# Kernel optimization log

Hardware: AMD Instinct MI355X
Metric: run time of the kernel (lower is better)

The kernel has to match this reference:

```python
import jax, jax.numpy as jnp
import numpy as np

HIDDEN = 128
HEADS = 8
HEAD_DIM = HIDDEN // HEADS


def setup_inputs() -> dict:
    key = jax.random.key(0)
    ks = jax.random.split(key, 10)
    B, V = 2, 768
    s = 1.0 / np.sqrt(HIDDEN)
    return {
        "x": jax.random.normal(ks[0], (B, V, HIDDEN), dtype=jnp.float32),
        "edge_gate": jax.random.uniform(ks[1], (B, V, V, HIDDEN), dtype=jnp.float32),
        "Wq": jax.random.normal(ks[2], (HIDDEN, HIDDEN), dtype=jnp.float32) * s,
        "bq": jnp.zeros((HIDDEN,), dtype=jnp.float32),
        "Wk": jax.random.normal(ks[3], (HIDDEN, HIDDEN), dtype=jnp.float32) * s,
        "bk": jnp.zeros((HIDDEN,), dtype=jnp.float32),
        "Wv": jax.random.normal(ks[4], (HIDDEN, HIDDEN), dtype=jnp.float32) * s,
        "bv": jnp.zeros((HIDDEN,), dtype=jnp.float32),
        "Wo": jax.random.normal(ks[5], (HIDDEN, HIDDEN), dtype=jnp.float32) * s,
        "bo": jnp.zeros((HIDDEN,), dtype=jnp.float32),
    }


def reference(x, edge_gate, Wq, bq, Wk, bk, Wv, bv, Wo, bo):
    B, V, H = x.shape
    nh, hd = HEADS, HEAD_DIM
    # torch Linear: y = x @ W.T + b
    q = (x @ Wq.T + bq).reshape(B, V, nh, hd).transpose(0, 2, 1, 3)  # (B,nh,V,hd)
    k = (x @ Wk.T + bk).reshape(B, V, nh, hd).transpose(0, 2, 1, 3)
    v = (x @ Wv.T + bv).reshape(B, V, nh, hd).transpose(0, 2, 1, 3)
    scores = jnp.einsum("bhqd,bhkd->bhqk", q, k) / jnp.sqrt(jnp.float32(hd))
    edge_mask = jnp.mean(edge_gate, axis=-1)[:, None]  # (B,1,V,V)
    weights = jax.nn.softmax(scores * edge_mask, axis=-1)
    attended = jnp.einsum("bhqk,bhkd->bhqd", weights, v)
    attended = attended.transpose(0, 2, 1, 3).reshape(B, V, H)
    return attended @ Wo.T + bo
```

## Files before the change

kernel.cpp:

```cpp
#include <hip/hip_runtime.h>
#include <math.h>

#define BB 2
#define VV 768
#define HID 128
#define NH 8
#define HD 16

#define QKV_BLOCKS 768
#define EDGE_BLOCKS 2048
#define EDGE_WAVES (EDGE_BLOCKS * 4)
#define NPAIR (BB * VV * VV / 2)
#define EDGE_ITERS (NPAIR / EDGE_WAVES)

__global__ __launch_bounds__(256) void fused_qkv_edgemean(
    const float* __restrict__ x, const float* __restrict__ eg,
    const float* __restrict__ Wq, const float* __restrict__ bq,
    const float* __restrict__ Wk, const float* __restrict__ bk,
    const float* __restrict__ Wv, const float* __restrict__ bv,
    float* __restrict__ qh, float* __restrict__ kh, float* __restrict__ vh,
    float* __restrict__ mask) {
    __shared__ float xs[2][HID];
    if (blockIdx.x < QKV_BLOCKS) {
        const int half = threadIdx.x >> 7;
        const int c    = threadIdx.x & 127;
        const int row  = blockIdx.x * 2 + half;
        xs[half][c] = x[row * HID + c];
        __syncthreads();
        const float4* xs4 = (const float4*)xs[half];
        const float4* wq4 = (const float4*)(Wq + c * HID);
        const float4* wk4 = (const float4*)(Wk + c * HID);
        const float4* wv4 = (const float4*)(Wv + c * HID);
        float aq = 0.f, ak = 0.f, av = 0.f;
#pragma unroll
        for (int k4 = 0; k4 < HID / 4; ++k4) {
            float4 xv = xs4[k4];
            float4 a = wq4[k4];
            aq += xv.x * a.x + xv.y * a.y + xv.z * a.z + xv.w * a.w;
            float4 bv2 = wk4[k4];
            ak += xv.x * bv2.x + xv.y * bv2.y + xv.z * bv2.z + xv.w * bv2.w;
            float4 cv = wv4[k4];
            av += xv.x * cv.x + xv.y * cv.y + xv.z * cv.z + xv.w * cv.w;
        }
        const int b = row / VV, vi = row - b * VV;
        const int idx = ((b * NH + (c >> 4)) * VV + vi) * HD + (c & 15);
        qh[idx] = aq + bq[c];
        kh[idx] = ak + bk[c];
        vh[idx] = av + bv[c];
    } else {
        const int lane = threadIdx.x & 63;
        const int w = (blockIdx.x - QKV_BLOCKS) * 4 + (threadIdx.x >> 6);
        const float4* eg4 = (const float4*)eg;
#pragma unroll 4
        for (int it = 0; it < EDGE_ITERS; ++it) {
            const int p = w + it * EDGE_WAVES;
            float4 v = eg4[(size_t)p * 64 + lane];
            float s = v.x + v.y + v.z + v.w;
            s += __shfl_xor(s, 1);
            s += __shfl_xor(s, 2);
            s += __shfl_xor(s, 4);
            s += __shfl_xor(s, 8);
            s += __shfl_xor(s, 16);
            if ((lane & 31) == 0)
                mask[p * 2 + (lane >> 5)] = s * (1.0f / 128.0f);
        }
    }
}

__global__ __launch_bounds__(256) void attn_kernel(
    const float* __restrict__ qh, const float* __restrict__ kh,
    const float* __restrict__ vh, const float* __restrict__ mask,
    float* __restrict__ att) {
    __shared__ float sc[4][VV];
    const int wid  = threadIdx.x >> 6;
    const int lane = threadIdx.x & 63;
    const int gw   = blockIdx.x * 4 + wid;
    const int qi   = gw % VV;
    const int bh   = gw / VV;
    const int b    = bh >> 3, h = bh & 7;

    const float4* qp = (const float4*)(qh + (size_t)(bh * VV + qi) * HD);
    const float4 q0 = qp[0], q1 = qp[1], q2 = qp[2], q3 = qp[3];

    const float* mrow  = mask + (size_t)(b * VV + qi) * VV;
    const float* kbase = kh + (size_t)bh * VV * HD;
    const float* vbase = vh + (size_t)bh * VV * HD;

    float m = -INFINITY;
#pragma unroll
    for (int t = 0; t < VV / 64; ++t) {
        const int j = lane + 64 * t;
        const float4* kp = (const float4*)(kbase + j * HD);
        float4 k0 = kp[0], k1 = kp[1], k2 = kp[2], k3 = kp[3];
        float dot = q0.x * k0.x + q0.y * k0.y + q0.z * k0.z + q0.w * k0.w
                  + q1.x * k1.x + q1.y * k1.y + q1.z * k1.z + q1.w * k1.w
                  + q2.x * k2.x + q2.y * k2.y + q2.z * k2.z + q2.w * k2.w
                  + q3.x * k3.x + q3.y * k3.y + q3.z * k3.z + q3.w * k3.w;
        float s = dot * 0.25f * mrow[j];
        sc[wid][j] = s;
        m = fmaxf(m, s);
    }
#pragma unroll
    for (int off = 1; off < 64; off <<= 1) m = fmaxf(m, __shfl_xor(m, off));

    float sum = 0.f;
    float acc[HD];
#pragma unroll
    for (int d = 0; d < HD; ++d) acc[d] = 0.f;
#pragma unroll
    for (int t = 0; t < VV / 64; ++t) {
        const int j = lane + 64 * t;
        float e = __expf(sc[wid][j] - m);
        sum += e;
        const float4* vp = (const float4*)(vbase + j * HD);
        float4 v0 = vp[0], v1 = vp[1], v2 = vp[2], v3 = vp[3];
        acc[0]  += e * v0.x; acc[1]  += e * v0.y; acc[2]  += e * v0.z; acc[3]  += e * v0.w;
        acc[4]  += e * v1.x; acc[5]  += e * v1.y; acc[6]  += e * v1.z; acc[7]  += e * v1.w;
        acc[8]  += e * v2.x; acc[9]  += e * v2.y; acc[10] += e * v2.z; acc[11] += e * v2.w;
        acc[12] += e * v3.x; acc[13] += e * v3.y; acc[14] += e * v3.z; acc[15] += e * v3.w;
    }
#pragma unroll
    for (int off = 1; off < 64; off <<= 1) sum += __shfl_xor(sum, off);

#pragma unroll
    for (int i = 0; i < 8; ++i) {
        float send = (lane & 1) ? acc[i] : acc[i + 8];
        float r = __shfl_xor(send, 1);
        acc[i] = ((lane & 1) ? acc[i + 8] : acc[i]) + r;
    }
#pragma unroll
    for (int i = 0; i < 4; ++i) {
        float send = (lane & 2) ? acc[i] : acc[i + 4];
        float r = __shfl_xor(send, 2);
        acc[i] = ((lane & 2) ? acc[i + 4] : acc[i]) + r;
    }
#pragma unroll
    for (int i = 0; i < 2; ++i) {
        float send = (lane & 4) ? acc[i] : acc[i + 2];
        float r = __shfl_xor(send, 4);
        acc[i] = ((lane & 4) ? acc[i + 2] : acc[i]) + r;
    }
    {
        float send = (lane & 8) ? acc[0] : acc[1];
        float r = __shfl_xor(send, 8);
        acc[0] = ((lane & 8) ? acc[1] : acc[0]) + r;
    }
    acc[0] += __shfl_xor(acc[0], 16);
    acc[0] += __shfl_xor(acc[0], 32);

    const float inv = 1.0f / sum;
    const int d = ((lane & 1) << 3) | ((lane & 2) << 1) | ((lane & 4) >> 1) | ((lane & 8) >> 3);
    if (lane < HD)
        att[(size_t)(b * VV + qi) * HID + h * HD + d] = acc[0] * inv;
}

__global__ __launch_bounds__(128) void outproj_kernel(
    const float* __restrict__ att, const float* __restrict__ Wo,
    const float* __restrict__ bo, float* __restrict__ out) {
    const int row = blockIdx.x;
    const int c   = threadIdx.x;
    __shared__ float xs[HID];
    xs[c] = att[row * HID + c];
    __syncthreads();
    const float4* xs4 = (const float4*)xs;
    const float4* wo4 = (const float4*)(Wo + c * HID);
    float a = 0.f;
#pragma unroll
    for (int k4 = 0; k4 < HID / 4; ++k4) {
        float4 xv = xs4[k4];
        float4 wv = wo4[k4];
        a += xv.x * wv.x + xv.y * wv.y + xv.z * wv.z + xv.w * wv.w;
    }
    out[row * HID + c] = a + bo[c];
}

extern "C" void kernel_launch(void* const* d_in, const int* in_sizes, int n_in,
                              void* d_out, int out_size, void* d_ws, size_t ws_size,
                              hipStream_t stream) {
    const float* x  = (const float*)d_in[0];
    const float* eg = (const float*)d_in[1];
    const float* Wq = (const float*)d_in[2];
    const float* bq = (const float*)d_in[3];
    const float* Wk = (const float*)d_in[4];
    const float* bk = (const float*)d_in[5];
    const float* Wv = (const float*)d_in[6];
    const float* bv = (const float*)d_in[7];
    const float* Wo = (const float*)d_in[8];
    const float* bo = (const float*)d_in[9];
    float* out = (float*)d_out;

    float* ws   = (float*)d_ws;
    float* mask = ws;
    float* qh   = mask + (size_t)BB * VV * VV;
    float* kh   = qh + (size_t)BB * VV * HID;
    float* vh   = kh + (size_t)BB * VV * HID;
    float* att  = vh + (size_t)BB * VV * HID;

    hipLaunchKernelGGL(fused_qkv_edgemean, dim3(QKV_BLOCKS + EDGE_BLOCKS), dim3(256), 0, stream,
                       x, eg, Wq, bq, Wk, bk, Wv, bv, qh, kh, vh, mask);
    hipLaunchKernelGGL(attn_kernel, dim3(BB * NH * VV / 4), dim3(256), 0, stream,
                       qh, kh, vh, mask, att);
    hipLaunchKernelGGL(outproj_kernel, dim3(BB * VV), dim3(128), 0, stream,
                       att, Wo, bo, out);
}
```

Measured before the change: 243.5 us.

## Process two queries per wave in attention and give each edge-mean wave a contiguous chunk

```diff
diff --git a/kernel.cpp b/kernel.cpp
--- a/kernel.cpp
+++ b/kernel.cpp
@@ -48,21 +48,23 @@
         kh[idx] = ak + bk[c];
         vh[idx] = av + bv[c];
     } else {
-        const int lane = threadIdx.x & 63;
+        const int l = threadIdx.x & 63;
         const int w = (blockIdx.x - QKV_BLOCKS) * 4 + (threadIdx.x >> 6);
         const float4* eg4 = (const float4*)eg;
+        const size_t wbase = (size_t)w * (EDGE_ITERS * 64);
 #pragma unroll 4
         for (int it = 0; it < EDGE_ITERS; ++it) {
-            const int p = w + it * EDGE_WAVES;
-            float4 v = eg4[(size_t)p * 64 + lane];
-            float s = v.x + v.y + v.z + v.w;
+            float4 v = eg4[wbase + it * 64 + l];
+            float s = (v.x + v.y) + (v.z + v.w);
             s += __shfl_xor(s, 1);
             s += __shfl_xor(s, 2);
             s += __shfl_xor(s, 4);
             s += __shfl_xor(s, 8);
             s += __shfl_xor(s, 16);
-            if ((lane & 31) == 0)
-                mask[p * 2 + (lane >> 5)] = s * (1.0f / 128.0f);
+            if ((l & 31) == 0) {
+                const int p = w * EDGE_ITERS + it;
+                mask[p * 2 + (l >> 5)] = s * (1.0f / 128.0f);
+            }
         }
     }
 }
@@ -71,87 +73,125 @@
     const float* __restrict__ qh, const float* __restrict__ kh,
     const float* __restrict__ vh, const float* __restrict__ mask,
     float* __restrict__ att) {
-    __shared__ float sc[4][VV];
+    __shared__ float sc[4][2][VV];
     const int wid  = threadIdx.x >> 6;
     const int lane = threadIdx.x & 63;
     const int gw   = blockIdx.x * 4 + wid;
-    const int qi   = gw % VV;
-    const int bh   = gw / VV;
+    const int pr   = gw % (VV / 2);
+    const int bh   = gw / (VV / 2);
     const int b    = bh >> 3, h = bh & 7;
-
-    const float4* qp = (const float4*)(qh + (size_t)(bh * VV + qi) * HD);
-    const float4 q0 = qp[0], q1 = qp[1], q2 = qp[2], q3 = qp[3];
-
-    const float* mrow  = mask + (size_t)(b * VV + qi) * VV;
+    const int q0i  = pr * 2, q1i = q0i + 1;
+
+    const float4* qp0 = (const float4*)(qh + ((size_t)bh * VV + q0i) * HD);
+    const float4 qa0 = qp0[0], qa1 = qp0[1], qa2 = qp0[2], qa3 = qp0[3];
+    const float4* qp1 = (const float4*)(qh + ((size_t)bh * VV + q1i) * HD);
+    const float4 qb0 = qp1[0], qb1 = qp1[1], qb2 = qp1[2], qb3 = qp1[3];
+
+    const float* mrow0 = mask + ((size_t)b * VV + q0i) * VV;
+    const float* mrow1 = mrow0 + VV;
     const float* kbase = kh + (size_t)bh * VV * HD;
     const float* vbase = vh + (size_t)bh * VV * HD;
 
-    float m = -INFINITY;
+    float m0 = -INFINITY, m1 = -INFINITY;
 #pragma unroll
     for (int t = 0; t < VV / 64; ++t) {
         const int j = lane + 64 * t;
         const float4* kp = (const float4*)(kbase + j * HD);
         float4 k0 = kp[0], k1 = kp[1], k2 = kp[2], k3 = kp[3];
-        float dot = q0.x * k0.x + q0.y * k0.y + q0.z * k0.z + q0.w * k0.w
-                  + q1.x * k1.x + q1.y * k1.y + q1.z * k1.z + q1.w * k1.w
-                  + q2.x * k2.x + q2.y * k2.y + q2.z * k2.z + q2.w * k2.w
-                  + q3.x * k3.x + q3.y * k3.y + q3.z * k3.z + q3.w * k3.w;
-        float s = dot * 0.25f * mrow[j];
-        sc[wid][j] = s;
-        m = fmaxf(m, s);
-    }
-#pragma unroll
-    for (int off = 1; off < 64; off <<= 1) m = fmaxf(m, __shfl_xor(m, off));
-
-    float sum = 0.f;
-    float acc[HD];
-#pragma unroll
-    for (int d = 0; d < HD; ++d) acc[d] = 0.f;
+        float d0 = qa0.x * k0.x + qa0.y * k0.y + qa0.z * k0.z + qa0.w * k0.w
+                 + qa1.x * k1.x + qa1.y * k1.y + qa1.z * k1.z + qa1.w * k1.w
+                 + qa2.x * k2.x + qa2.y * k2.y + qa2.z * k2.z + qa2.w * k2.w
+                 + qa3.x * k3.x + qa3.y * k3.y + qa3.z * k3.z + qa3.w * k3.w;
+        float d1 = qb0.x * k0.x + qb0.y * k0.y + qb0.z * k0.z + qb0.w * k0.w
+                 + qb1.x * k1.x + qb1.y * k1.y + qb1.z * k1.z + qb1.w * k1.w
+                 + qb2.x * k2.x + qb2.y * k2.y + qb2.z * k2.z + qb2.w * k2.w
+                 + qb3.x * k3.x + qb3.y * k3.y + qb3.z * k3.z + qb3.w * k3.w;
+        float s0 = d0 * 0.25f * mrow0[j];
+        float s1 = d1 * 0.25f * mrow1[j];
+        sc[wid][0][j] = s0;
+        sc[wid][1][j] = s1;
+        m0 = fmaxf(m0, s0);
+        m1 = fmaxf(m1, s1);
+    }
+#pragma unroll
+    for (int off = 1; off < 64; off <<= 1) {
+        m0 = fmaxf(m0, __shfl_xor(m0, off));
+        m1 = fmaxf(m1, __shfl_xor(m1, off));
+    }
+
+    float sum0 = 0.f, sum1 = 0.f;
+    float acc0[HD], acc1[HD];
+#pragma unroll
+    for (int d = 0; d < HD; ++d) { acc0[d] = 0.f; acc1[d] = 0.f; }
 #pragma unroll
     for (int t = 0; t < VV / 64; ++t) {
         const int j = lane + 64 * t;
-        float e = __expf(sc[wid][j] - m);
-        sum += e;
+        float e0 = __expf(sc[wid][0][j] - m0);
+        float e1 = __expf(sc[wid][1][j] - m1);
+        sum0 += e0;
+        sum1 += e1;
         const float4* vp = (const float4*)(vbase + j * HD);
         float4 v0 = vp[0], v1 = vp[1], v2 = vp[2], v3 = vp[3];
-        acc[0]  += e * v0.x; acc[1]  += e * v0.y; acc[2]  += e * v0.z; acc[3]  += e * v0.w;
-        acc[4]  += e * v1.x; acc[5]  += e * v1.y; acc[6]  += e * v1.z; acc[7]  += e * v1.w;
-        acc[8]  += e * v2.x; acc[9]  += e * v2.y; acc[10] += e * v2.z; acc[11] += e * v2.w;
-        acc[12] += e * v3.x; acc[13] += e * v3.y; acc[14] += e * v3.z; acc[15] += e * v3.w;
-    }
-#pragma unroll
-    for (int off = 1; off < 64; off <<= 1) sum += __shfl_xor(sum, off);
+        acc0[0]  += e0 * v0.x; acc0[1]  += e0 * v0.y; acc0[2]  += e0 * v0.z; acc0[3]  += e0 * v0.w;
+        acc0[4]  += e0 * v1.x; acc0[5]  += e0 * v1.y; acc0[6]  += e0 * v1.z; acc0[7]  += e0 * v1.w;
+        acc0[8]  += e0 * v2.x; acc0[9]  += e0 * v2.y; acc0[10] += e0 * v2.z; acc0[11] += e0 * v2.w;
+        acc0[12] += e0 * v3.x; acc0[13] += e0 * v3.y; acc0[14] += e0 * v3.z; acc0[15] += e0 * v3.w;
+        acc1[0]  += e1 * v0.x; acc1[1]  += e1 * v0.y; acc1[2]  += e1 * v0.z; acc1[3]  += e1 * v0.w;
+        acc1[4]  += e1 * v1.x; acc1[5]  += e1 * v1.y; acc1[6]  += e1 * v1.z; acc1[7]  += e1 * v1.w;
+        acc1[8]  += e1 * v2.x; acc1[9]  += e1 * v2.y; acc1[10] += e1 * v2.z; acc1[11] += e1 * v2.w;
+        acc1[12] += e1 * v3.x; acc1[13] += e1 * v3.y; acc1[14] += e1 * v3.z; acc1[15] += e1 * v3.w;
+    }
+#pragma unroll
+    for (int off = 1; off < 64; off <<= 1) {
+        sum0 += __shfl_xor(sum0, off);
+        sum1 += __shfl_xor(sum1, off);
+    }
 
 #pragma unroll
     for (int i = 0; i < 8; ++i) {
-        float send = (lane & 1) ? acc[i] : acc[i + 8];
-        float r = __shfl_xor(send, 1);
-        acc[i] = ((lane & 1) ? acc[i + 8] : acc[i]) + r;
+        float sa = (lane & 1) ? acc0[i] : acc0[i + 8];
+        float ra = __shfl_xor(sa, 1);
+        acc0[i] = ((lane & 1) ? acc0[i + 8] : acc0[i]) + ra;
+        float sb = (lane & 1) ? acc1[i] : acc1[i + 8];
+        float rb = __shfl_xor(sb, 1);
+        acc1[i] = ((lane & 1) ? acc1[i + 8] : acc1[i]) + rb;
     }
 #pragma unroll
     for (int i = 0; i < 4; ++i) {
-        float send = (lane & 2) ? acc[i] : acc[i + 4];
-        float r = __shfl_xor(send, 2);
-        acc[i] = ((lane & 2) ? acc[i + 4] : acc[i]) + r;
+        float sa = (lane & 2) ? acc0[i] : acc0[i + 4];
+        float ra = __shfl_xor(sa, 2);
+        acc0[i] = ((lane & 2) ? acc0[i + 4] : acc0[i]) + ra;
+        float sb = (lane & 2) ? acc1[i] : acc1[i + 4];
+        float rb = __shfl_xor(sb, 2);
+        acc1[i] = ((lane & 2) ? acc1[i + 4] : acc1[i]) + rb;
     }
 #pragma unroll
     for (int i = 0; i < 2; ++i) {
-        float send = (lane & 4) ? acc[i] : acc[i + 2];
-        float r = __shfl_xor(send, 4);
-        acc[i] = ((lane & 4) ? acc[i + 2] : acc[i]) + r;
+        float sa = (lane & 4) ? acc0[i] : acc0[i + 2];
+        float ra = __shfl_xor(sa, 4);
+        acc0[i] = ((lane & 4) ? acc0[i + 2] : acc0[i]) + ra;
+        float sb = (lane & 4) ? acc1[i] : acc1[i + 2];
+        float rb = __shfl_xor(sb, 4);
+        acc1[i] = ((lane & 4) ? acc1[i + 2] : acc1[i]) + rb;
     }
     {
-        float send = (lane & 8) ? acc[0] : acc[1];
-        float r = __shfl_xor(send, 8);
-        acc[0] = ((lane & 8) ? acc[1] : acc[0]) + r;
-    }
-    acc[0] += __shfl_xor(acc[0], 16);
-    acc[0] += __shfl_xor(acc[0], 32);
-
-    const float inv = 1.0f / sum;
+        float sa = (lane & 8) ? acc0[0] : acc0[1];
+        float ra = __shfl_xor(sa, 8);
+        acc0[0] = ((lane & 8) ? acc0[1] : acc0[0]) + ra;
+        float sb = (lane & 8) ? acc1[0] : acc1[1];
+        float rb = __shfl_xor(sb, 8);
+        acc1[0] = ((lane & 8) ? acc1[1] : acc1[0]) + rb;
+    }
+    acc0[0] += __shfl_xor(acc0[0], 16);
+    acc0[0] += __shfl_xor(acc0[0], 32);
+    acc1[0] += __shfl_xor(acc1[0], 16);
+    acc1[0] += __shfl_xor(acc1[0], 32);
+
     const int d = ((lane & 1) << 3) | ((lane & 2) << 1) | ((lane & 4) >> 1) | ((lane & 8) >> 3);
-    if (lane < HD)
-        att[(size_t)(b * VV + qi) * HID + h * HD + d] = acc[0] * inv;
+    if (lane < HD) {
+        att[((size_t)b * VV + q0i) * HID + h * HD + d] = acc0[0] / sum0;
+        att[((size_t)b * VV + q1i) * HID + h * HD + d] = acc1[0] / sum1;
+    }
 }
 
 __global__ __launch_bounds__(128) void outproj_kernel(
@@ -198,7 +238,7 @@
 
     hipLaunchKernelGGL(fused_qkv_edgemean, dim3(QKV_BLOCKS + EDGE_BLOCKS), dim3(256), 0, stream,
                        x, eg, Wq, bq, Wk, bk, Wv, bv, qh, kh, vh, mask);
-    hipLaunchKernelGGL(attn_kernel, dim3(BB * NH * VV / 4), dim3(256), 0, stream,
+    hipLaunchKernelGGL(attn_kernel, dim3(BB * NH * VV / 8), dim3(256), 0, stream,
                        qh, kh, vh, mask, att);
     hipLaunchKernelGGL(outproj_kernel, dim3(BB * VV), dim3(128), 0, stream,
                        att, Wo, bo, out);
```

Measured after the change: 219.3 us (median of 2 runs). 10.0% less time.

## Fuse edge-mean, attention and output projection into one per-query kernel

Applied to the files above, without the earlier changes.

```diff
diff --git a/kernel.cpp b/kernel.cpp
--- a/kernel.cpp
+++ b/kernel.cpp
@@ -7,171 +7,182 @@
 #define NH 8
 #define HD 16
 
-#define QKV_BLOCKS 768
-#define EDGE_BLOCKS 2048
-#define EDGE_WAVES (EDGE_BLOCKS * 4)
-#define NPAIR (BB * VV * VV / 2)
-#define EDGE_ITERS (NPAIR / EDGE_WAVES)
-
-__global__ __launch_bounds__(256) void fused_qkv_edgemean(
-    const float* __restrict__ x, const float* __restrict__ eg,
+typedef float f4v __attribute__((ext_vector_type(4)));
+
+__global__ __launch_bounds__(256) void qkv_kernel(
+    const float* __restrict__ x,
     const float* __restrict__ Wq, const float* __restrict__ bq,
     const float* __restrict__ Wk, const float* __restrict__ bk,
     const float* __restrict__ Wv, const float* __restrict__ bv,
-    float* __restrict__ qh, float* __restrict__ kh, float* __restrict__ vh,
-    float* __restrict__ mask) {
+    float* __restrict__ qh, float* __restrict__ kh, float* __restrict__ vh) {
     __shared__ float xs[2][HID];
-    if (blockIdx.x < QKV_BLOCKS) {
-        const int half = threadIdx.x >> 7;
-        const int c    = threadIdx.x & 127;
-        const int row  = blockIdx.x * 2 + half;
-        xs[half][c] = x[row * HID + c];
-        __syncthreads();
-        const float4* xs4 = (const float4*)xs[half];
-        const float4* wq4 = (const float4*)(Wq + c * HID);
-        const float4* wk4 = (const float4*)(Wk + c * HID);
-        const float4* wv4 = (const float4*)(Wv + c * HID);
-        float aq = 0.f, ak = 0.f, av = 0.f;
-#pragma unroll
-        for (int k4 = 0; k4 < HID / 4; ++k4) {
-            float4 xv = xs4[k4];
-            float4 a = wq4[k4];
-            aq += xv.x * a.x + xv.y * a.y + xv.z * a.z + xv.w * a.w;
-            float4 bv2 = wk4[k4];
-            ak += xv.x * bv2.x + xv.y * bv2.y + xv.z * bv2.z + xv.w * bv2.w;
-            float4 cv = wv4[k4];
-            av += xv.x * cv.x + xv.y * cv.y + xv.z * cv.z + xv.w * cv.w;
-        }
-        const int b = row / VV, vi = row - b * VV;
-        const int idx = ((b * NH + (c >> 4)) * VV + vi) * HD + (c & 15);
-        qh[idx] = aq + bq[c];
-        kh[idx] = ak + bk[c];
-        vh[idx] = av + bv[c];
-    } else {
-        const int lane = threadIdx.x & 63;
-        const int w = (blockIdx.x - QKV_BLOCKS) * 4 + (threadIdx.x >> 6);
-        const float4* eg4 = (const float4*)eg;
-#pragma unroll 4
-        for (int it = 0; it < EDGE_ITERS; ++it) {
-            const int p = w + it * EDGE_WAVES;
-            float4 v = eg4[(size_t)p * 64 + lane];
-            float s = v.x + v.y + v.z + v.w;
-            s += __shfl_xor(s, 1);
-            s += __shfl_xor(s, 2);
-            s += __shfl_xor(s, 4);
-            s += __shfl_xor(s, 8);
-            s += __shfl_xor(s, 16);
-            if ((lane & 31) == 0)
-                mask[p * 2 + (lane >> 5)] = s * (1.0f / 128.0f);
-        }
-    }
-}
-
-__global__ __launch_bounds__(256) void attn_kernel(
-    const float* __restrict__ qh, const float* __restrict__ kh,
-    const float* __restrict__ vh, const float* __restrict__ mask,
-    float* __restrict__ att) {
-    __shared__ float sc[4][VV];
-    const int wid  = threadIdx.x >> 6;
-    const int lane = threadIdx.x & 63;
-    const int gw   = blockIdx.x * 4 + wid;
-    const int qi   = gw % VV;
-    const int bh   = gw / VV;
-    const int b    = bh >> 3, h = bh & 7;
-
-    const float4* qp = (const float4*)(qh + (size_t)(bh * VV + qi) * HD);
-    const float4 q0 = qp[0], q1 = qp[1], q2 = qp[2], q3 = qp[3];
-
-    const float* mrow  = mask + (size_t)(b * VV + qi) * VV;
-    const float* kbase = kh + (size_t)bh * VV * HD;
-    const float* vbase = vh + (size_t)bh * VV * HD;
-
-    float m = -INFINITY;
-#pragma unroll
-    for (int t = 0; t < VV / 64; ++t) {
-        const int j = lane + 64 * t;
-        const float4* kp = (const float4*)(kbase + j * HD);
-        float4 k0 = kp[0], k1 = kp[1], k2 = kp[2], k3 = kp[3];
-        float dot = q0.x * k0.x + q0.y * k0.y + q0.z * k0.z + q0.w * k0.w
-                  + q1.x * k1.x + q1.y * k1.y + q1.z * k1.z + q1.w * k1.w
-                  + q2.x * k2.x + q2.y * k2.y + q2.z * k2.z + q2.w * k2.w
-                  + q3.x * k3.x + q3.y * k3.y + q3.z * k3.z + q3.w * k3.w;
-        float s = dot * 0.25f * mrow[j];
-        sc[wid][j] = s;
-        m = fmaxf(m, s);
-    }
-#pragma unroll
-    for (int off = 1; off < 64; off <<= 1) m = fmaxf(m, __shfl_xor(m, off));
-
-    float sum = 0.f;
-    float acc[HD];
-#pragma unroll
-    for (int d = 0; d < HD; ++d) acc[d] = 0.f;
-#pragma unroll
-    for (int t = 0; t < VV / 64; ++t) {
-        const int j = lane + 64 * t;
-        float e = __expf(sc[wid][j] - m);
-        sum += e;
-        const float4* vp = (const float4*)(vbase + j * HD);
-        float4 v0 = vp[0], v1 = vp[1], v2 = vp[2], v3 = vp[3];
-        acc[0]  += e * v0.x; acc[1]  += e * v0.y; acc[2]  += e * v0.z; acc[3]  += e * v0.w;
-        acc[4]  += e * v1.x; acc[5]  += e * v1.y; acc[6]  += e * v1.z; acc[7]  += e * v1.w;
-        acc[8]  += e * v2.x; acc[9]  += e * v2.y; acc[10] += e * v2.z; acc[11] += e * v2.w;
-        acc[12] += e * v3.x; acc[13] += e * v3.y; acc[14] += e * v3.z; acc[15] += e * v3.w;
-    }
-#pragma unroll
-    for (int off = 1; off < 64; off <<= 1) sum += __shfl_xor(sum, off);
-
-#pragma unroll
-    for (int i = 0; i < 8; ++i) {
-        float send = (lane & 1) ? acc[i] : acc[i + 8];
-        float r = __shfl_xor(send, 1);
-        acc[i] = ((lane & 1) ? acc[i + 8] : acc[i]) + r;
-    }
-#pragma unroll
-    for (int i = 0; i < 4; ++i) {
-        float send = (lane & 2) ? acc[i] : acc[i + 4];
-        float r = __shfl_xor(send, 2);
-        acc[i] = ((lane & 2) ? acc[i + 4] : acc[i]) + r;
-    }
-#pragma unroll
-    for (int i = 0; i < 2; ++i) {
-        float send = (lane & 4) ? acc[i] : acc[i + 2];
-        float r = __shfl_xor(send, 4);
-        acc[i] = ((lane & 4) ? acc[i + 2] : acc[i]) + r;
-    }
-    {
-        float send = (lane & 8) ? acc[0] : acc[1];
-        float r = __shfl_xor(send, 8);
-        acc[0] = ((lane & 8) ? acc[1] : acc[0]) + r;
-    }
-    acc[0] += __shfl_xor(acc[0], 16);
-    acc[0] += __shfl_xor(acc[0], 32);
-
-    const float inv = 1.0f / sum;
-    const int d = ((lane & 1) << 3) | ((lane & 2) << 1) | ((lane & 4) >> 1) | ((lane & 8) >> 3);
-    if (lane < HD)
-        att[(size_t)(b * VV + qi) * HID + h * HD + d] = acc[0] * inv;
-}
-
-__global__ __launch_bounds__(128) void outproj_kernel(
-    const float* __restrict__ att, const float* __restrict__ Wo,
-    const float* __restrict__ bo, float* __restrict__ out) {
-    const int row = blockIdx.x;
-    const int c   = threadIdx.x;
-    __shared__ float xs[HID];
-    xs[c] = att[row * HID + c];
+    const int half = threadIdx.x >> 7;
+    const int c    = threadIdx.x & 127;
+    const int row  = blockIdx.x * 2 + half;
+    xs[half][c] = x[row * HID + c];
     __syncthreads();
-    const float4* xs4 = (const float4*)xs;
-    const float4* wo4 = (const float4*)(Wo + c * HID);
-    float a = 0.f;
+    const float4* xs4 = (const float4*)xs[half];
+    const float4* wq4 = (const float4*)(Wq + c * HID);
+    const float4* wk4 = (const float4*)(Wk + c * HID);
+    const float4* wv4 = (const float4*)(Wv + c * HID);
+    float aq = 0.f, ak = 0.f, av = 0.f;
 #pragma unroll
     for (int k4 = 0; k4 < HID / 4; ++k4) {
         float4 xv = xs4[k4];
-        float4 wv = wo4[k4];
-        a += xv.x * wv.x + xv.y * wv.y + xv.z * wv.z + xv.w * wv.w;
-    }
-    out[row * HID + c] = a + bo[c];
+        float4 a = wq4[k4];
+        aq += xv.x * a.x + xv.y * a.y + xv.z * a.z + xv.w * a.w;
+        float4 bv2 = wk4[k4];
+        ak += xv.x * bv2.x + xv.y * bv2.y + xv.z * bv2.z + xv.w * bv2.w;
+        float4 cv = wv4[k4];
+        av += xv.x * cv.x + xv.y * cv.y + xv.z * cv.z + xv.w * cv.w;
+    }
+    const int b = row / VV, vi = row - b * VV;
+    const int idx = ((b * NH + (c >> 4)) * VV + vi) * HD + (c & 15);
+    qh[idx] = aq + bq[c];
+    kh[idx] = ak + bk[c];
+    vh[idx] = av + bv[c];
+}
+
+__global__ __launch_bounds__(256) void fused_edge_attn_out(
+    const float* __restrict__ eg,
+    const float* __restrict__ qh, const float* __restrict__ kh,
+    const float* __restrict__ vh,
+    const float* __restrict__ Wo, const float* __restrict__ bo,
+    float* __restrict__ out) {
+    __shared__ float mask_lds[VV];
+    __shared__ float sc_lds[4][VV];
+    __shared__ float att_lds[HID];
+
+    const int lane = threadIdx.x & 63;
+    const int wid  = threadIdx.x >> 6;
+    const int bq   = blockIdx.x;
+    const int b    = bq / VV, q = bq - b * VV;
+
+    {
+        const float* wbase = eg + (size_t)bq * (VV * HID) + wid * (192 * HID);
+#pragma unroll 1
+        for (int batch = 0; batch < 12; ++batch) {
+            const float* p0 = wbase + batch * 2048 + lane * 4;
+            const float* p1 = p0 + 1024;
+            f4v v0, v1, v2, v3, v4, v5, v6, v7;
+            asm volatile(
+                "global_load_dwordx4 %0, %8, off sc0 nt\n\t"
+                "global_load_dwordx4 %1, %8, off offset:1024 sc0 nt\n\t"
+                "global_load_dwordx4 %2, %8, off offset:2048 sc0 nt\n\t"
+                "global_load_dwordx4 %3, %8, off offset:3072 sc0 nt\n\t"
+                "global_load_dwordx4 %4, %9, off sc0 nt\n\t"
+                "global_load_dwordx4 %5, %9, off offset:1024 sc0 nt\n\t"
+                "global_load_dwordx4 %6, %9, off offset:2048 sc0 nt\n\t"
+                "global_load_dwordx4 %7, %9, off offset:3072 sc0 nt\n\t"
+                "s_waitcnt vmcnt(0)"
+                : "=&v"(v0), "=&v"(v1), "=&v"(v2), "=&v"(v3),
+                  "=&v"(v4), "=&v"(v5), "=&v"(v6), "=&v"(v7)
+                : "v"(p0), "v"(p1));
+            const int rbase = wid * 192 + batch * 16 + (lane >> 5);
+            float s;
+#define REDUCE_ROW(vi, i)                                                  \
+            s = ((vi[0] + vi[1]) + (vi[2] + vi[3]));                       \
+            s += __shfl_xor(s, 1);  s += __shfl_xor(s, 2);                 \
+            s += __shfl_xor(s, 4);  s += __shfl_xor(s, 8);                 \
+            s += __shfl_xor(s, 16);                                        \
+            if ((lane & 31) == 0)                                          \
+                mask_lds[rbase + 2 * (i)] = s * (1.0f / 128.0f);
+            REDUCE_ROW(v0, 0) REDUCE_ROW(v1, 1) REDUCE_ROW(v2, 2) REDUCE_ROW(v3, 3)
+            REDUCE_ROW(v4, 4) REDUCE_ROW(v5, 5) REDUCE_ROW(v6, 6) REDUCE_ROW(v7, 7)
+#undef REDUCE_ROW
+        }
+    }
+    __syncthreads();
+
+#pragma unroll 1
+    for (int hh = 0; hh < 2; ++hh) {
+        const int h  = wid * 2 + hh;
+        const int bh = b * NH + h;
+        const float4* qp = (const float4*)(qh + ((size_t)bh * VV + q) * HD);
+        const float4 q0 = qp[0], q1 = qp[1], q2 = qp[2], q3 = qp[3];
+        const float* kbase = kh + (size_t)bh * VV * HD;
+        const float* vbase = vh + (size_t)bh * VV * HD;
+
+        float m = -INFINITY;
+#pragma unroll
+        for (int t = 0; t < VV / 64; ++t) {
+            const int j = lane + 64 * t;
+            const float4* kp = (const float4*)(kbase + j * HD);
+            float4 k0 = kp[0], k1 = kp[1], k2 = kp[2], k3 = kp[3];
+            float dot = q0.x * k0.x + q0.y * k0.y + q0.z * k0.z + q0.w * k0.w
+                      + q1.x * k1.x + q1.y * k1.y + q1.z * k1.z + q1.w * k1.w
+                      + q2.x * k2.x + q2.y * k2.y + q2.z * k2.z + q2.w * k2.w
+                      + q3.x * k3.x + q3.y * k3.y + q3.z * k3.z + q3.w * k3.w;
+            float s = dot * 0.25f * mask_lds[j];
+            sc_lds[wid][j] = s;
+            m = fmaxf(m, s);
+        }
+#pragma unroll
+        for (int off = 1; off < 64; off <<= 1) m = fmaxf(m, __shfl_xor(m, off));
+
+        float sum = 0.f;
+        float acc[HD];
+#pragma unroll
+        for (int d = 0; d < HD; ++d) acc[d] = 0.f;
+#pragma unroll
+        for (int t = 0; t < VV / 64; ++t) {
+            const int j = lane + 64 * t;
+            float e = __expf(sc_lds[wid][j] - m);
+            sum += e;
+            const float4* vp = (const float4*)(vbase + j * HD);
+            float4 v0 = vp[0], v1 = vp[1], v2 = vp[2], v3 = vp[3];
+            acc[0]  += e * v0.x; acc[1]  += e * v0.y; acc[2]  += e * v0.z; acc[3]  += e * v0.w;
+            acc[4]  += e * v1.x; acc[5]  += e * v1.y; acc[6]  += e * v1.z; acc[7]  += e * v1.w;
+            acc[8]  += e * v2.x; acc[9]  += e * v2.y; acc[10] += e * v2.z; acc[11] += e * v2.w;
+            acc[12] += e * v3.x; acc[13] += e * v3.y; acc[14] += e * v3.z; acc[15] += e * v3.w;
+        }
+#pragma unroll
+        for (int off = 1; off < 64; off <<= 1) sum += __shfl_xor(sum, off);
+
+#pragma unroll
+        for (int i = 0; i < 8; ++i) {
+            float send = (lane & 1) ? acc[i] : acc[i + 8];
+            float r = __shfl_xor(send, 1);
+            acc[i] = ((lane & 1) ? acc[i + 8] : acc[i]) + r;
+        }
+#pragma unroll
+        for (int i = 0; i < 4; ++i) {
+            float send = (lane & 2) ? acc[i] : acc[i + 4];
+            float r = __shfl_xor(send, 2);
+            acc[i] = ((lane & 2) ? acc[i + 4] : acc[i]) + r;
+        }
+#pragma unroll
+        for (int i = 0; i < 2; ++i) {
+            float send = (lane & 4) ? acc[i] : acc[i + 2];
+            float r = __shfl_xor(send, 4);
+            acc[i] = ((lane & 4) ? acc[i + 2] : acc[i]) + r;
+        }
+        {
+            float send = (lane & 8) ? acc[0] : acc[1];
+            float r = __shfl_xor(send, 8);
+            acc[0] = ((lane & 8) ? acc[1] : acc[0]) + r;
+        }
+        acc[0] += __shfl_xor(acc[0], 16);
+        acc[0] += __shfl_xor(acc[0], 32);
+
+        const int d = ((lane & 1) << 3) | ((lane & 2) << 1) | ((lane & 4) >> 1) | ((lane & 8) >> 3);
+        if (lane < HD) att_lds[h * HD + d] = acc[0] / sum;
+    }
+    __syncthreads();
+
+    if (threadIdx.x < HID) {
+        const int c = threadIdx.x;
+        const float4* a4 = (const float4*)att_lds;
+        const float4* w4 = (const float4*)(Wo + c * HID);
+        float a = 0.f;
+#pragma unroll
+        for (int k4 = 0; k4 < HID / 4; ++k4) {
+            float4 xv = a4[k4];
+            float4 wv = w4[k4];
+            a += xv.x * wv.x + xv.y * wv.y + xv.z * wv.z + xv.w * wv.w;
+        }
+        out[(size_t)bq * HID + c] = a + bo[c];
+    }
 }
 
 extern "C" void kernel_launch(void* const* d_in, const int* in_sizes, int n_in,
@@ -189,17 +200,13 @@
     const float* bo = (const float*)d_in[9];
     float* out = (float*)d_out;
 
-    float* ws   = (float*)d_ws;
-    float* mask = ws;
-    float* qh   = mask + (size_t)BB * VV * VV;
-    float* kh   = qh + (size_t)BB * VV * HID;
-    float* vh   = kh + (size_t)BB * VV * HID;
-    float* att  = vh + (size_t)BB * VV * HID;
-
-    hipLaunchKernelGGL(fused_qkv_edgemean, dim3(QKV_BLOCKS + EDGE_BLOCKS), dim3(256), 0, stream,
-                       x, eg, Wq, bq, Wk, bk, Wv, bv, qh, kh, vh, mask);
-    hipLaunchKernelGGL(attn_kernel, dim3(BB * NH * VV / 4), dim3(256), 0, stream,
-                       qh, kh, vh, mask, att);
-    hipLaunchKernelGGL(outproj_kernel, dim3(BB * VV), dim3(128), 0, stream,
-                       att, Wo, bo, out);
+    float* ws = (float*)d_ws;
+    float* qh = ws;
+    float* kh = qh + (size_t)BB * VV * HID;
+    float* vh = kh + (size_t)BB * VV * HID;
+
+    hipLaunchKernelGGL(qkv_kernel, dim3(BB * VV / 2), dim3(256), 0, stream,
+                       x, Wq, bq, Wk, bk, Wv, bv, qh, kh, vh);
+    hipLaunchKernelGGL(fused_edge_attn_out, dim3(BB * VV), dim3(256), 0, stream,
+                       eg, qh, kh, vh, Wo, bo, out);
 }
```

New measurement: 265.0 us. +8.8%, slower.
